# Optimization experiments

Hardware: AMD Instinct MI355X
Metric: run time of the kernel (lower is better)

Reference implementation:

```python
import jax, jax.numpy as jnp
import numpy as np

B, T, D = 2, 2048, 2048
N_HEADS, N_KV, HEAD_DIM = 8, 4, 256
S_CACHE = 2048
WINDOW = 512
SOFT_CAP = 50.0
ROPE_TS = 10000
ROPE_PROP = 1.0
EPS = 1e-6
NEG_INF = -2.3819763e38


def setup_inputs() -> dict:
    key = jax.random.key(0)
    ks = jax.random.split(key, 6)
    x = jax.random.normal(ks[0], (B, T, D), dtype=jnp.float32)
    wq = jax.random.normal(ks[1], (D, N_HEADS * HEAD_DIM), dtype=jnp.float32) * (D ** -0.5)
    wk = jax.random.normal(ks[2], (D, N_KV * HEAD_DIM), dtype=jnp.float32) * (D ** -0.5)
    wv = jax.random.normal(ks[3], (D, N_KV * HEAD_DIM), dtype=jnp.float32) * (D ** -0.5)
    wo = jax.random.normal(ks[4], (N_HEADS * HEAD_DIM, D), dtype=jnp.float32) * ((N_HEADS * HEAD_DIM) ** -0.5)
    return {
        'x': x,
        'segment_pos': jnp.broadcast_to(jnp.arange(T, dtype=jnp.int32), (B, T)),
        'cur_ind': 0,
        'wq': wq, 'wk': wk, 'wv': wv, 'wo': wo,
        'q_norm_scale': jnp.zeros((HEAD_DIM,), jnp.float32),
        'k_norm_scale': jnp.zeros((HEAD_DIM,), jnp.float32),
        'k_cache': jnp.zeros((B, S_CACHE, N_KV, HEAD_DIM), jnp.float32),
        'v_cache': jnp.zeros((B, S_CACHE, N_KV, HEAD_DIM), jnp.float32),
    }


def _rms_norm(x, scale, eps=EPS):
    # Gemma4RMSNorm: fp32 norm, (1 + scale) offset
    xf = x.astype(jnp.float32)
    n = xf * jax.lax.rsqrt(jnp.mean(jnp.square(xf), -1, keepdims=True) + eps)
    return (n * (1.0 + scale)).astype(x.dtype)


def _apply_rope(x, pos, max_timescale=ROPE_TS, proportion=ROPE_PROP):
    # x: [B, T, n, H]; pos: [B, T]. Partial RoPE on first proportion*H dims.
    H = x.shape[-1]
    rope_dim = int(H * proportion)
    half = rope_dim // 2
    frac = jnp.arange(half, dtype=jnp.float32) / half
    timescale = jnp.asarray(max_timescale, jnp.float32) ** frac  # [half]
    sinusoid = pos.astype(jnp.float32)[..., None] / timescale    # [B, T, half]
    sin = jnp.sin(sinusoid)[:, :, None, :]
    cos = jnp.cos(sinusoid)[:, :, None, :]
    x_rope, x_pass = x[..., :rope_dim], x[..., rope_dim:]
    x1, x2 = x_rope[..., :half], x_rope[..., half:]
    rotated = jnp.concatenate([x1 * cos - x2 * sin, x2 * cos + x1 * sin], axis=-1)
    return jnp.concatenate([rotated, x_pass], axis=-1).astype(x.dtype)


def reference(x, segment_pos, cur_ind, wq, wk, wv, wo, q_norm_scale, k_norm_scale, k_cache, v_cache):
    b, t, _ = x.shape
    g = N_HEADS // N_KV  # GQA group size

    q = (x @ wq).reshape(b, t, N_HEADS, HEAD_DIM)
    k = (x @ wk).reshape(b, t, N_KV, HEAD_DIM)
    v = (x @ wv).reshape(b, t, N_KV, HEAD_DIM)

    # QK-norm (per-head RMSNorm) then RoPE
    q = _rms_norm(q, q_norm_scale)
    k = _rms_norm(k, k_norm_scale)
    q = _apply_rope(q, segment_pos)
    k = _apply_rope(k, segment_pos)

    # KV-cache scatter write at cur_ind
    idx = jnp.asarray(cur_ind, jnp.int32)
    k_cache = jax.lax.dynamic_update_slice(k_cache, k, (0, idx, 0, 0))
    v_cache = jax.lax.dynamic_update_slice(v_cache, v, (0, idx, 0, 0))

    # Attention logits over full cache: [b, kv, g, t, s]
    qg = q.reshape(b, t, N_KV, g, HEAD_DIM) * (HEAD_DIM ** -0.5)
    logits = jnp.einsum('btkgh,bskh->bkgts', qg, k_cache)
    logits = SOFT_CAP * jnp.tanh(logits / SOFT_CAP)

    # Causal + sliding-window mask from absolute positions
    q_pos = segment_pos[:, :, None]                              # [b, t, 1]
    k_pos = jnp.arange(S_CACHE, dtype=jnp.int32)[None, None, :]  # [1, 1, s]
    mask = (k_pos <= q_pos) & (q_pos - k_pos < WINDOW)           # [b, t, s]
    logits = jnp.where(mask[:, None, None, :, :], logits, NEG_INF)

    probs = jax.nn.softmax(logits, axis=-1)
    attn = jnp.einsum('bkgts,bskh->btkgh', probs, v_cache).reshape(b, t, N_HEADS * HEAD_DIM)
    return attn @ wo
```

## Files before the change

kernel.cpp:

```cpp
#include <hip/hip_runtime.h>

#define T_SEQ 2048
#define NHEADS 8
#define NKV 4
#define HD 256
#define WIN 512

typedef __bf16 bf16x8 __attribute__((ext_vector_type(8)));
typedef float f32x4 __attribute__((ext_vector_type(4)));

__device__ __forceinline__ float bf2f(unsigned short u) {
    return __uint_as_float(((unsigned int)u) << 16);
}
__device__ __forceinline__ unsigned short f2bf(float f) {
    unsigned int u = __float_as_uint(f);
    u += 0x7fffu + ((u >> 16) & 1u);
    return (unsigned short)(u >> 16);
}

#define GLOAD_LDS16(gptr, lptr)                                            \
    __builtin_amdgcn_global_load_lds(                                      \
        (const __attribute__((address_space(1))) unsigned int*)(gptr),     \
        (__attribute__((address_space(3))) unsigned int*)(lptr), 16, 0, 0)

__global__ void detect_dtype(const unsigned short* __restrict__ x, int* flag) {
    int tid = threadIdx.x;
    int cnt = 0;
    for (int i = 0; i < 64; ++i) {
        unsigned short u = x[2 * (tid * 64 + i)];
        int e = (u >> 7) & 0xFF;
        cnt += (e >= 100 && e <= 140) ? 1 : 0;
    }
    #pragma unroll
    for (int o = 32; o >= 1; o >>= 1) cnt += __shfl_xor(cnt, o);
    if (tid == 0) *flag = (cnt > 2048) ? 1 : 0;
}

__global__ __launch_bounds__(256) void convert_to_bf16(
    const void* __restrict__ src, unsigned short* __restrict__ dst,
    const int* __restrict__ flag, int n)
{
    int i = (blockIdx.x * 256 + threadIdx.x) * 8;
    if (i >= n) return;
    if (*flag) {
        *(uint4*)&dst[i] = *(const uint4*)((const unsigned short*)src + i);
    } else {
        const float* s = (const float*)src + i;
        unsigned short v[8];
        #pragma unroll
        for (int j = 0; j < 8; ++j) v[j] = f2bf(s[j]);
        *(uint4*)&dst[i] = *(uint4*)v;
    }
}

__global__ __launch_bounds__(256) void transpose_cvt(
    const void* __restrict__ src, unsigned short* __restrict__ dst,
    const int* __restrict__ flag, int R, int C)
{
    __shared__ unsigned short tile[32][33];
    const int t = threadIdx.x;
    const int c = t & 31, r8 = t >> 5;
    const int bx = blockIdx.x, by = blockIdx.y;
    const int isb = *flag;
    #pragma unroll
    for (int i = 0; i < 4; ++i) {
        int r = r8 + i * 8;
        size_t idx = (size_t)(by * 32 + r) * C + bx * 32 + c;
        tile[r][c] = isb ? ((const unsigned short*)src)[idx]
                         : f2bf(((const float*)src)[idx]);
    }
    __syncthreads();
    #pragma unroll
    for (int i = 0; i < 4; ++i) {
        int r = r8 + i * 8;
        dst[(size_t)(bx * 32 + r) * R + by * 32 + c] = tile[c][r];
    }
}

__global__ __launch_bounds__(256) void transpose_qkv_w(
    const void* __restrict__ wq, const void* __restrict__ wk,
    const void* __restrict__ wv, unsigned short* __restrict__ dst,
    const int* __restrict__ flag)
{
    __shared__ unsigned short tile[32][33];
    const int t = threadIdx.x;
    const int c = t & 31, r8 = t >> 5;
    const int bx = blockIdx.x, by = blockIdx.y;
    const void* src; int C, rowoff, cb;
    if (bx < 64)      { src = wq; C = 2048; rowoff = 0;    cb = bx; }
    else if (bx < 96) { src = wk; C = 1024; rowoff = 2048; cb = bx - 64; }
    else              { src = wv; C = 1024; rowoff = 3072; cb = bx - 96; }
    const int isb = *flag;
    #pragma unroll
    for (int i = 0; i < 4; ++i) {
        int r = r8 + i * 8;
        size_t idx = (size_t)(by * 32 + r) * C + cb * 32 + c;
        tile[r][c] = isb ? ((const unsigned short*)src)[idx]
                         : f2bf(((const float*)src)[idx]);
    }
    __syncthreads();
    #pragma unroll
    for (int i = 0; i < 4; ++i) {
        int r = r8 + i * 8;
        dst[(size_t)(rowoff + cb * 32 + r) * 2048 + by * 32 + c] = tile[c][r];
    }
}

__global__ __launch_bounds__(256) void gemm_bf16(
    const unsigned short* __restrict__ A,
    const unsigned short* __restrict__ Bt,
    void* __restrict__ C,
    int M, int Ntot, int K, int n_base,
    const int* __restrict__ flag, int force_bf16)
{
    __shared__ __align__(16) unsigned short As[128 * 32];
    __shared__ __align__(16) unsigned short Bs[128 * 32];
    const int tid = threadIdx.x;
    const int n0 = blockIdx.x * 128;
    const int m0 = blockIdx.y * 128;
    const int wave = tid >> 6;
    const int lane = tid & 63;
    const int wm = (wave >> 1) * 64;
    const int wn = (wave & 1) * 64;
    const int quad = lane >> 4;
    const int l16 = lane & 15;
    const int obf = force_bf16 | *flag;

    f32x4 acc[4][4];
    #pragma unroll
    for (int i = 0; i < 4; ++i)
        #pragma unroll
        for (int j = 0; j < 4; ++j)
            acc[i][j] = f32x4{0.f, 0.f, 0.f, 0.f};

    for (int kk = 0; kk < K; kk += 32) {
        #pragma unroll
        for (int i = 0; i < 2; ++i) {
            int ch = tid + i * 256;
            int row = ch >> 2;
            int ko = (ch & 3) * 8;
            GLOAD_LDS16(&A[(size_t)(m0 + row) * K + kk + ko],  &As[ch * 8]);
            GLOAD_LDS16(&Bt[(size_t)(n0 + row) * K + kk + ko], &Bs[ch * 8]);
        }
        __syncthreads();
        bf16x8 af[4], bfr[4];
        #pragma unroll
        for (int mi = 0; mi < 4; ++mi)
            af[mi] = *(const bf16x8*)&As[(wm + mi * 16 + l16) * 32 + quad * 8];
        #pragma unroll
        for (int ni = 0; ni < 4; ++ni)
            bfr[ni] = *(const bf16x8*)&Bs[(wn + ni * 16 + l16) * 32 + quad * 8];
        #pragma unroll
        for (int mi = 0; mi < 4; ++mi)
            #pragma unroll
            for (int ni = 0; ni < 4; ++ni)
                acc[mi][ni] = __builtin_amdgcn_mfma_f32_16x16x32_bf16(
                    af[mi], bfr[ni], acc[mi][ni], 0, 0, 0);
        __syncthreads();
    }

    #pragma unroll
    for (int mi = 0; mi < 4; ++mi)
        #pragma unroll
        for (int ni = 0; ni < 4; ++ni)
            #pragma unroll
            for (int r = 0; r < 4; ++r) {
                int row = m0 + wm + mi * 16 + quad * 4 + r;
                int col = n_base + n0 + wn + ni * 16 + l16;
                size_t idx = (size_t)row * Ntot + col;
                if (obf) ((unsigned short*)C)[idx] = f2bf(acc[mi][ni][r]);
                else     ((float*)C)[idx]          = acc[mi][ni][r];
            }
}

__global__ __launch_bounds__(512, 2) void gemm256_bf16(
    const unsigned short* __restrict__ A,
    const unsigned short* __restrict__ Bt,
    void* __restrict__ C,
    int M, int Ntot, int K, int n_base, int gx,
    const int* __restrict__ flag, int force_bf16)
{
    __shared__ __align__(16) unsigned short A_lds[2][256 * 64];
    __shared__ __align__(16) unsigned short B_lds[2][256 * 64];

    const int tid = threadIdx.x;
    const int cpx = gridDim.x >> 3;
    const int swzb = (blockIdx.x & 7) * cpx + (blockIdx.x >> 3);
    const int bx = swzb % gx, by = swzb / gx;
    const int n0 = bx * 256, m0 = by * 256;

    const int wave = tid >> 6, lane = tid & 63;
    const int wr = wave >> 2, wc = wave & 3;
    const int quad = lane >> 4, l16 = lane & 15;
    const int sw7 = l16 & 7;
    const int obf = force_bf16 | *flag;

    const int trow = tid >> 3;
    const int tg   = tid & 7;
    const int tsw  = (tg ^ (trow & 7)) * 8;

    f32x4 acc[8][4];
    #pragma unroll
    for (int i = 0; i < 8; ++i)
        #pragma unroll
        for (int j = 0; j < 4; ++j)
            acc[i][j] = f32x4{0.f, 0.f, 0.f, 0.f};

    const int NT = K >> 6;
    const int NI = NT >> 1;

#define STAGE_A(d_, hm_, kt_)                                                  \
    do { _Pragma("unroll") for (int j = 0; j < 2; ++j) {                       \
        int r_ = j * 128 + (hm_) * 64 + trow;                                  \
        GLOAD_LDS16(&A[(size_t)(m0 + r_) * K + (kt_) * 64 + tsw],              \
                    &A_lds[d_][((hm_) * 128 + j * 64 + trow) * 64 + tg * 8]);  \
    } } while (0)

#define STAGE_B(d_, hn_, kt_)                                                  \
    do { _Pragma("unroll") for (int j = 0; j < 2; ++j) {                       \
        int w2_ = j * 64 + trow;                                               \
        int r_ = (w2_ >> 5) * 64 + (hn_) * 32 + (w2_ & 31);                    \
        GLOAD_LDS16(&Bt[(size_t)(n0 + r_) * K + (kt_) * 64 + tsw],             \
                    &B_lds[d_][((hn_) * 128 + w2_) * 64 + tg * 8]);            \
    } } while (0)

    bf16x8 a[4][2], b0[2][2], b1[2][2];

#define LDA_H(d_, hm_)                                                         \
    do { _Pragma("unroll") for (int mi = 0; mi < 4; ++mi)                      \
         _Pragma("unroll") for (int ks = 0; ks < 2; ++ks)                      \
            a[mi][ks] = *(const bf16x8*)&A_lds[d_][                            \
                ((hm_) * 128 + wr * 64 + mi * 16 + l16) * 64                   \
                + (((ks * 4 + quad) ^ sw7) * 8)]; } while (0)

#define LDB_H(d_, hn_, bb_)                                                    \
    do { _Pragma("unroll") for (int ni = 0; ni < 2; ++ni)                      \
         _Pragma("unroll") for (int ks = 0; ks < 2; ++ks)                      \
            bb_[ni][ks] = *(const bf16x8*)&B_lds[d_][                          \
                ((hn_) * 128 + wc * 32 + ni * 16 + l16) * 64                   \
                + (((ks * 4 + quad) ^ sw7) * 8)]; } while (0)

#define MFMAQ(hm_, hn_, bb_)                                                   \
    do { __builtin_amdgcn_s_setprio(1);                                        \
         _Pragma("unroll") for (int mi = 0; mi < 4; ++mi)                      \
         _Pragma("unroll") for (int ni = 0; ni < 2; ++ni)                      \
         _Pragma("unroll") for (int ks = 0; ks < 2; ++ks)                      \
            acc[(hm_) * 4 + mi][(hn_) * 2 + ni] =                              \
                __builtin_amdgcn_mfma_f32_16x16x32_bf16(                       \
                    a[mi][ks], bb_[ni][ks],                                    \
                    acc[(hm_) * 4 + mi][(hn_) * 2 + ni], 0, 0, 0);             \
         __builtin_amdgcn_s_setprio(0); } while (0)

#define BAR() do { __builtin_amdgcn_sched_barrier(0);                          \
                   __builtin_amdgcn_s_barrier();                               \
                   __builtin_amdgcn_sched_barrier(0); } while (0)
#define LGKM0() do { asm volatile("s_waitcnt lgkmcnt(0)" ::: "memory");        \
                     __builtin_amdgcn_sched_barrier(0); } while (0)
#define VMC(n_) asm volatile("s_waitcnt vmcnt(" #n_ ")" ::: "memory")

    STAGE_A(0, 0, 0); STAGE_B(0, 0, 0); STAGE_B(0, 1, 0); STAGE_A(0, 1, 0);
    STAGE_A(1, 0, 1); STAGE_B(1, 0, 1); STAGE_B(1, 1, 1);
    VMC(6);
    BAR();

    for (int i = 0; i < NI; ++i) {
        const int t2 = 2 * i + 2, t3 = 2 * i + 3;
        const bool s2 = t2 < NT, s3 = t3 < NT;

        LDA_H(0, 0); LDB_H(0, 0, b0);
        STAGE_A(1, 1, 2 * i + 1);
        BAR(); LGKM0(); MFMAQ(0, 0, b0);
        BAR();
        LDB_H(0, 1, b1);
        if (s2) STAGE_A(0, 0, t2);
        BAR(); LGKM0(); MFMAQ(0, 1, b1);
        BAR();
        LDA_H(0, 1);
        if (s2) STAGE_B(0, 0, t2);
        BAR(); LGKM0(); MFMAQ(1, 1, b1);
        BAR();
        if (s2) STAGE_B(0, 1, t2);
        BAR(); LGKM0(); MFMAQ(1, 0, b0);
        if (s2) { VMC(6); } else { VMC(0); }
        BAR();
        LDA_H(1, 0); LDB_H(1, 0, b0);
        if (s2) STAGE_A(0, 1, t2);
        BAR(); LGKM0(); MFMAQ(0, 0, b0);
        BAR();
        LDB_H(1, 1, b1);
        if (s3) STAGE_A(1, 0, t3);
        BAR(); LGKM0(); MFMAQ(0, 1, b1);
        BAR();
        LDA_H(1, 1);
        if (s3) STAGE_B(1, 0, t3);
        BAR(); LGKM0(); MFMAQ(1, 1, b1);
        BAR();
        if (s3) STAGE_B(1, 1, t3);
        BAR(); LGKM0(); MFMAQ(1, 0, b0);
        if (s3) { VMC(6); } else { VMC(0); }
        BAR();
    }

#undef STAGE_A
#undef STAGE_B
#undef LDA_H
#undef LDB_H
#undef MFMAQ
#undef BAR
#undef LGKM0
#undef VMC

    #pragma unroll
    for (int mi = 0; mi < 8; ++mi)
        #pragma unroll
        for (int ni = 0; ni < 4; ++ni)
            #pragma unroll
            for (int r = 0; r < 4; ++r) {
                int row = m0 + wr * 128 + mi * 16 + quad * 4 + r;
                int col = n_base + n0 + wc * 64 + ni * 16 + l16;
                size_t idx = (size_t)row * Ntot + col;
                if (obf) ((unsigned short*)C)[idx] = f2bf(acc[mi][ni][r]);
                else     ((float*)C)[idx]          = acc[mi][ni][r];
            }
}

__global__ __launch_bounds__(256) void finalize_qk(
    unsigned short* __restrict__ qkv,
    const int* __restrict__ segment_pos,
    const void* __restrict__ qs_raw,
    const void* __restrict__ ks_raw,
    const int* __restrict__ flag)
{
    const int w = blockIdx.x * 4 + (threadIdx.x >> 6);
    const int lane = threadIdx.x & 63;
    const int b = w / (T_SEQ * 12);
    const int rem = w % (T_SEQ * 12);
    const int t = rem / 12;
    const int slot = rem % 12;
    const bool isq = slot < 8;
    const int col0 = isq ? slot * 256 : 2048 + (slot - 8) * 256;
    unsigned short* p = qkv + (size_t)(b * T_SEQ + t) * 4096 + col0;
    const int isb = *flag;

    float e[4];
    #pragma unroll
    for (int j = 0; j < 4; ++j) e[j] = bf2f(p[lane + 64 * j]);
    float ss = e[0] * e[0] + e[1] * e[1] + e[2] * e[2] + e[3] * e[3];
    #pragma unroll
    for (int o = 32; o >= 1; o >>= 1) ss += __shfl_xor(ss, o);
    const float rn = rsqrtf(ss * (1.0f / 256.0f) + 1e-6f);
    const void* scp = isq ? qs_raw : ks_raw;
    float nrm[4];
    #pragma unroll
    for (int j = 0; j < 4; ++j) {
        float sc = isb ? bf2f(((const unsigned short*)scp)[lane + 64 * j])
                       : ((const float*)scp)[lane + 64 * j];
        nrm[j] = e[j] * rn * (1.0f + sc);
    }

    const int pos = segment_pos[b * T_SEQ + t];
    #pragma unroll
    for (int pp = 0; pp < 2; ++pp) {
        const int i = lane + 64 * pp;
        const float inv_ts = __expf((float)i * -0.07195578415606293f);
        float s, c;
        __sincosf((float)pos * inv_ts, &s, &c);
        const float x1 = nrm[pp], x2 = nrm[pp + 2];
        p[i]       = f2bf(x1 * c - x2 * s);
        p[i + 128] = f2bf(x2 * c + x1 * s);
    }
}

__global__ __launch_bounds__(256) void build_vt(
    const unsigned short* __restrict__ qkv, unsigned short* __restrict__ vt)
{
    __shared__ unsigned short tile[32][33];
    const int bkv = blockIdx.z;
    const int b = bkv >> 2, kv = bkv & 3;
    const int s0 = blockIdx.x * 32, d0 = blockIdx.y * 32;
    const int c = threadIdx.x & 31, r8 = threadIdx.x >> 5;
    #pragma unroll
    for (int i = 0; i < 4; ++i) {
        int r = r8 + i * 8;
        tile[r][c] = qkv[(size_t)(b * T_SEQ + s0 + r) * 4096 + 3072 + kv * 256 + d0 + c];
    }
    __syncthreads();
    #pragma unroll
    for (int i = 0; i < 4; ++i) {
        int r = r8 + i * 8;
        vt[((size_t)bkv * 256 + d0 + r) * T_SEQ + s0 + c] = tile[c][r];
    }
}

#define PSTR 80
__global__ __launch_bounds__(256, 2) void attn_mfma(
    const unsigned short* __restrict__ qkv,
    const unsigned short* __restrict__ vt,
    unsigned short* __restrict__ out)
{
    __shared__ __align__(16) unsigned short SMEM[16384 + 16384 + 4 * 16 * PSTR];
    unsigned short* K_lds  = SMEM;
    unsigned short* VT_lds = SMEM + 16384;

    const int tid = threadIdx.x;
    const int wave = tid >> 6, lane = tid & 63;
    const int l16 = lane & 15, quad = lane >> 4;
    const int sw = l16 & 7;
    const int bkv = blockIdx.x & 7;
    const int qt  = blockIdx.x >> 3;
    const int b = bkv >> 2, kvh = bkv & 3;
    const int t0 = qt * 32;
    const int h = kvh * 2 + (wave >> 1);
    const int woff = (wave & 1) * 16;
    const int tq = t0 + woff + l16;
    unsigned short* P_lds = SMEM + 32768 + wave * 16 * PSTR;

    bf16x8 qf[8];
    {
        const unsigned short* qp =
            qkv + (size_t)(b * T_SEQ + tq) * 4096 + h * 256 + quad * 8;
        #pragma unroll
        for (int c = 0; c < 8; ++c) qf[c] = *(const bf16x8*)(qp + 32 * c);
    }

    f32x4 o[16];
    #pragma unroll
    for (int nt = 0; nt < 16; ++nt) o[nt] = f32x4{0.f, 0.f, 0.f, 0.f};
    float l_run = 0.f;

    int s_lo = t0 - (WIN - 1); if (s_lo < 0) s_lo = 0;
    const int s_base = s_lo & ~63;
    const int s_last = t0 + 31;
    const int tqmin = t0 + woff;
    const int tqmax = tqmin + 15;
    const int wlo   = tqmin - (WIN - 1);
    const size_t kgbase = (size_t)b * T_SEQ * 4096 + 2048 + kvh * 256;
    const size_t vgbase = (size_t)bkv * 256 * T_SEQ;

    for (int sb = s_base; sb <= s_last; sb += 64) {
        __syncthreads();

        #pragma unroll
        for (int i = 0; i < 8; ++i) {
            int ch = tid + 256 * i;
            int row = ch >> 5, e8 = ch & 31;
            GLOAD_LDS16(&qkv[kgbase + (size_t)(sb + row) * 4096
                             + ((e8 ^ (row & 7)) * 8)],
                        &K_lds[ch * 8]);
        }
        #pragma unroll
        for (int i = 0; i < 8; ++i) {
            int ch = tid + 256 * i;
            int dr = ch >> 3, e8 = ch & 7;
            GLOAD_LDS16(&vt[vgbase + (size_t)dr * T_SEQ + sb
                            + ((e8 ^ (dr & 7)) * 8)],
                        &VT_lds[ch * 8]);
        }
        __syncthreads();

        if (sb > tqmax || sb + 63 < wlo) continue;

        f32x4 st[4];
        #pragma unroll
        for (int mt = 0; mt < 4; ++mt) st[mt] = f32x4{0.f, 0.f, 0.f, 0.f};
        __builtin_amdgcn_s_setprio(1);
        #pragma unroll
        for (int c = 0; c < 8; ++c) {
            bf16x8 kf[4];
            #pragma unroll
            for (int mt = 0; mt < 4; ++mt)
                kf[mt] = *(const bf16x8*)&K_lds[(mt * 16 + l16) * 256 + (((4 * c + quad) ^ sw) * 8)];
            #pragma unroll
            for (int mt = 0; mt < 4; ++mt)
                st[mt] = __builtin_amdgcn_mfma_f32_16x16x32_bf16(kf[mt], qf[c], st[mt], 0, 0, 0);
        }
        __builtin_amdgcn_s_setprio(0);

        #pragma unroll
        for (int mt = 0; mt < 4; ++mt)
            #pragma unroll
            for (int r = 0; r < 4; ++r) {
                int sp = sb + mt * 16 + quad * 4 + r;
                float e2 = __expf(st[mt][r] * 0.0025f);
                float p = __expf(20.0f - 100.0f / (e2 + 1.0f));
                bool valid = (sp <= tq) && (tq - sp < WIN);
                p = valid ? p : 0.0f;
                l_run += p;
                P_lds[l16 * PSTR + mt * 16 + quad * 4 + r] = f2bf(p);
            }

        #pragma unroll
        for (int c = 0; c < 2; ++c) {
            bf16x8 pf = *(const bf16x8*)&P_lds[l16 * PSTR + 32 * c + quad * 8];
            __builtin_amdgcn_s_setprio(1);
            #pragma unroll
            for (int nt = 0; nt < 16; ++nt) {
                bf16x8 vf = *(const bf16x8*)&VT_lds[(nt * 16 + l16) * 64 + (((4 * c + quad) ^ sw) * 8)];
                o[nt] = __builtin_amdgcn_mfma_f32_16x16x32_bf16(pf, vf, o[nt], 0, 0, 0);
            }
            __builtin_amdgcn_s_setprio(0);
        }
    }

    l_run += __shfl_xor(l_run, 16);
    l_run += __shfl_xor(l_run, 32);
    float linv[4];
    #pragma unroll
    for (int r = 0; r < 4; ++r) linv[r] = 1.0f / __shfl(l_run, quad * 4 + r);

    __syncthreads();
    unsigned short* W = SMEM + wave * (16 * 264);
    #pragma unroll
    for (int nt = 0; nt < 16; ++nt)
        #pragma unroll
        for (int r = 0; r < 4; ++r)
            W[(quad * 4 + r) * 264 + nt * 16 + l16] = f2bf(o[nt][r] * linv[r]);
    const int lr = lane >> 2, lc = (lane & 3) * 64;
    unsigned short* ob = out + (size_t)(b * T_SEQ + t0 + woff + lr) * 2048 + h * 256 + lc;
    #pragma unroll
    for (int j = 0; j < 8; ++j)
        *(uint4*)(ob + j * 8) = *(const uint4*)&W[lr * 264 + lc + j * 8];
}

extern "C" void kernel_launch(void* const* d_in, const int* in_sizes, int n_in,
                              void* d_out, int out_size, void* d_ws, size_t ws_size,
                              hipStream_t stream) {
    const void* x   = d_in[0];
    const int*  sp  = (const int*)d_in[1];
    const void* wq  = d_in[3];
    const void* wk  = d_in[4];
    const void* wv  = d_in[5];
    const void* wo  = d_in[6];
    const void* qsc = d_in[7];
    const void* ksc = d_in[8];

    unsigned short* ws = (unsigned short*)d_ws;
    int*            flag = (int*)ws;
    unsigned short* qkv  = (unsigned short*)d_out;
    dim3 blk(256);

    const size_t NEED = (size_t)(2048 + 8388608 + 8388608) * sizeof(unsigned short);

    detect_dtype<<<1, 64, 0, stream>>>((const unsigned short*)x, flag);

    if (ws_size >= NEED) {
        unsigned short* xhat = ws + 2048;
        unsigned short* wT   = xhat + (size_t)4096 * 2048;
        unsigned short* abuf = xhat;
        unsigned short* vtb  = wT;
        unsigned short* woT  = wT + (size_t)2048 * 2048;

        convert_to_bf16<<<4096, blk, 0, stream>>>(x, xhat, flag, 4096 * 2048);

        transpose_qkv_w<<<dim3(128, 64), blk, 0, stream>>>(wq, wk, wv, wT, flag);

        gemm256_bf16<<<256, 512, 0, stream>>>(xhat, wT, qkv,
                                              4096, 4096, 2048, 0, 16, flag, 1);

        finalize_qk<<<12288, blk, 0, stream>>>(qkv, sp, qsc, ksc, flag);

        build_vt<<<dim3(64, 8, 8), blk, 0, stream>>>(qkv, vtb);
        attn_mfma<<<512, blk, 0, stream>>>(qkv, vtb, abuf);

        transpose_cvt<<<dim3(64, 64), blk, 0, stream>>>(wo, woT, flag, 2048, 2048);
        gemm256_bf16<<<128, 512, 0, stream>>>(abuf, woT, d_out,
                                              4096, 2048, 2048, 0, 8, flag, 0);
    } else {
        unsigned short* reg1 = ws + 2048;
        unsigned short* reg2 = reg1 + (size_t)4096 * 2048;
        unsigned short* xhat = reg1;
        unsigned short* abuf = reg1;

        convert_to_bf16<<<4096, blk, 0, stream>>>(x, xhat, flag, 4096 * 2048);

        transpose_cvt<<<dim3(64, 64), blk, 0, stream>>>(wq, reg2, flag, 2048, 2048);
        gemm_bf16<<<dim3(16, 32), blk, 0, stream>>>(xhat, reg2, qkv,
                                                    4096, 4096, 2048, 0, flag, 1);
        transpose_cvt<<<dim3(32, 64), blk, 0, stream>>>(wk, reg2,                     flag, 2048, 1024);
        transpose_cvt<<<dim3(32, 64), blk, 0, stream>>>(wv, reg2 + (size_t)1024*2048, flag, 2048, 1024);
        gemm_bf16<<<dim3(16, 32), blk, 0, stream>>>(xhat, reg2, qkv,
                                                    4096, 4096, 2048, 2048, flag, 1);

        finalize_qk<<<12288, blk, 0, stream>>>(qkv, sp, qsc, ksc, flag);

        build_vt<<<dim3(64, 8, 8), blk, 0, stream>>>(qkv, reg2);
        attn_mfma<<<512, blk, 0, stream>>>(qkv, reg2, abuf);

        transpose_cvt<<<dim3(64, 64), blk, 0, stream>>>(wo, reg2, flag, 2048, 2048);
        gemm_bf16<<<dim3(16, 32), blk, 0, stream>>>(abuf, reg2, d_out,
                                                    4096, 2048, 2048, 0, flag, 0);
    }
}
```

Before: 359.1 us.

## Fuse prep/post kernels and overlap V loads with QK compute in attention

Merges the input conversion with the QKV weight transpose into one launch. It also merges QK-norm/RoPE, the V transpose and the wo transpose into a second launch, cutting kernel launches and tail effects between small kernels. In the attention loop, the kernel now waits only for the K tile (partial vmcnt) before computing QK logits, and waits for the V tile later. This lets V global-to-LDS loads overlap the QK MFMAs and softmax. Inactive tiles now still run the barriers. Correctness depends on the vmcnt count matching the load issue order.

```diff
diff --git a/kernel.cpp b/kernel.cpp
--- a/kernel.cpp
+++ b/kernel.cpp
@@ -36,13 +36,10 @@
     if (tid == 0) *flag = (cnt > 2048) ? 1 : 0;
 }
 
-__global__ __launch_bounds__(256) void convert_to_bf16(
-    const void* __restrict__ src, unsigned short* __restrict__ dst,
-    const int* __restrict__ flag, int n)
-{
-    int i = (blockIdx.x * 256 + threadIdx.x) * 8;
-    if (i >= n) return;
-    if (*flag) {
+__device__ __forceinline__ void dev_convert8(
+    const void* src, unsigned short* dst, int isb, int i)
+{
+    if (isb) {
         *(uint4*)&dst[i] = *(const uint4*)((const unsigned short*)src + i);
     } else {
         const float* s = (const float*)src + i;
@@ -53,15 +50,11 @@
     }
 }
 
-__global__ __launch_bounds__(256) void transpose_cvt(
-    const void* __restrict__ src, unsigned short* __restrict__ dst,
-    const int* __restrict__ flag, int R, int C)
-{
-    __shared__ unsigned short tile[32][33];
-    const int t = threadIdx.x;
-    const int c = t & 31, r8 = t >> 5;
-    const int bx = blockIdx.x, by = blockIdx.y;
-    const int isb = *flag;
+__device__ __forceinline__ void dev_transpose32(
+    const void* src, unsigned short* dst, int isb, int R, int C,
+    int bx, int by, int tid, unsigned short (*tile)[33])
+{
+    const int c = tid & 31, r8 = tid >> 5;
     #pragma unroll
     for (int i = 0; i < 4; ++i) {
         int r = r8 + i * 8;
@@ -77,32 +70,150 @@
     }
 }
 
-__global__ __launch_bounds__(256) void transpose_qkv_w(
-    const void* __restrict__ wq, const void* __restrict__ wk,
-    const void* __restrict__ wv, unsigned short* __restrict__ dst,
-    const int* __restrict__ flag)
-{
-    __shared__ unsigned short tile[32][33];
-    const int t = threadIdx.x;
-    const int c = t & 31, r8 = t >> 5;
-    const int bx = blockIdx.x, by = blockIdx.y;
-    const void* src; int C, rowoff, cb;
-    if (bx < 64)      { src = wq; C = 2048; rowoff = 0;    cb = bx; }
-    else if (bx < 96) { src = wk; C = 1024; rowoff = 2048; cb = bx - 64; }
-    else              { src = wv; C = 1024; rowoff = 3072; cb = bx - 96; }
-    const int isb = *flag;
+__device__ __forceinline__ void dev_finalize(
+    unsigned short* qkv, const int* segment_pos,
+    const void* qs_raw, const void* ks_raw, int isb, int w, int lane)
+{
+    const int b = w / (T_SEQ * 12);
+    const int rem = w % (T_SEQ * 12);
+    const int t = rem / 12;
+    const int slot = rem % 12;
+    const bool isq = slot < 8;
+    const int col0 = isq ? slot * 256 : 2048 + (slot - 8) * 256;
+    unsigned short* p = qkv + (size_t)(b * T_SEQ + t) * 4096 + col0;
+
+    float e[4];
+    #pragma unroll
+    for (int j = 0; j < 4; ++j) e[j] = bf2f(p[lane + 64 * j]);
+    float ss = e[0] * e[0] + e[1] * e[1] + e[2] * e[2] + e[3] * e[3];
+    #pragma unroll
+    for (int o = 32; o >= 1; o >>= 1) ss += __shfl_xor(ss, o);
+    const float rn = rsqrtf(ss * (1.0f / 256.0f) + 1e-6f);
+    const void* scp = isq ? qs_raw : ks_raw;
+    float nrm[4];
+    #pragma unroll
+    for (int j = 0; j < 4; ++j) {
+        float sc = isb ? bf2f(((const unsigned short*)scp)[lane + 64 * j])
+                       : ((const float*)scp)[lane + 64 * j];
+        nrm[j] = e[j] * rn * (1.0f + sc);
+    }
+
+    const int pos = segment_pos[b * T_SEQ + t];
+    #pragma unroll
+    for (int pp = 0; pp < 2; ++pp) {
+        const int i = lane + 64 * pp;
+        const float inv_ts = __expf((float)i * -0.07195578415606293f);
+        float s, c;
+        __sincosf((float)pos * inv_ts, &s, &c);
+        const float x1 = nrm[pp], x2 = nrm[pp + 2];
+        p[i]       = f2bf(x1 * c - x2 * s);
+        p[i + 128] = f2bf(x2 * c + x1 * s);
+    }
+}
+
+__device__ __forceinline__ void dev_build_vt(
+    const unsigned short* qkv, unsigned short* vt,
+    int bx, int by, int bz, int tid, unsigned short (*tile)[33])
+{
+    const int bkv = bz;
+    const int b = bkv >> 2, kv = bkv & 3;
+    const int s0 = bx * 32, d0 = by * 32;
+    const int c = tid & 31, r8 = tid >> 5;
     #pragma unroll
     for (int i = 0; i < 4; ++i) {
         int r = r8 + i * 8;
-        size_t idx = (size_t)(by * 32 + r) * C + cb * 32 + c;
-        tile[r][c] = isb ? ((const unsigned short*)src)[idx]
-                         : f2bf(((const float*)src)[idx]);
+        tile[r][c] = qkv[(size_t)(b * T_SEQ + s0 + r) * 4096 + 3072 + kv * 256 + d0 + c];
     }
     __syncthreads();
     #pragma unroll
     for (int i = 0; i < 4; ++i) {
         int r = r8 + i * 8;
-        dst[(size_t)(rowoff + cb * 32 + r) * 2048 + by * 32 + c] = tile[c][r];
+        vt[((size_t)bkv * 256 + d0 + r) * T_SEQ + s0 + c] = tile[c][r];
+    }
+}
+
+__global__ __launch_bounds__(256) void convert_to_bf16(
+    const void* __restrict__ src, unsigned short* __restrict__ dst,
+    const int* __restrict__ flag, int n)
+{
+    int i = (blockIdx.x * 256 + threadIdx.x) * 8;
+    if (i >= n) return;
+    dev_convert8(src, dst, *flag, i);
+}
+
+__global__ __launch_bounds__(256) void transpose_cvt(
+    const void* __restrict__ src, unsigned short* __restrict__ dst,
+    const int* __restrict__ flag, int R, int C)
+{
+    __shared__ unsigned short tile[32][33];
+    dev_transpose32(src, dst, *flag, R, C, blockIdx.x, blockIdx.y,
+                    threadIdx.x, tile);
+}
+
+__global__ __launch_bounds__(256) void finalize_qk(
+    unsigned short* __restrict__ qkv,
+    const int* __restrict__ segment_pos,
+    const void* __restrict__ qs_raw,
+    const void* __restrict__ ks_raw,
+    const int* __restrict__ flag)
+{
+    dev_finalize(qkv, segment_pos, qs_raw, ks_raw, *flag,
+                 blockIdx.x * 4 + (threadIdx.x >> 6), threadIdx.x & 63);
+}
+
+__global__ __launch_bounds__(256) void build_vt(
+    const unsigned short* __restrict__ qkv, unsigned short* __restrict__ vt)
+{
+    __shared__ unsigned short tile[32][33];
+    dev_build_vt(qkv, vt, blockIdx.x, blockIdx.y, blockIdx.z,
+                 threadIdx.x, tile);
+}
+
+__global__ __launch_bounds__(256) void prep_fused(
+    const void* __restrict__ x,
+    const void* __restrict__ wq, const void* __restrict__ wk,
+    const void* __restrict__ wv,
+    unsigned short* __restrict__ xhat, unsigned short* __restrict__ wT,
+    const int* __restrict__ flag)
+{
+    __shared__ unsigned short tile[32][33];
+    const int bid = blockIdx.x;
+    const int tid = threadIdx.x;
+    const int isb = *flag;
+    if (bid < 4096) {
+        dev_convert8(x, xhat, isb, (bid * 256 + tid) * 8);
+    } else {
+        const int k = bid - 4096;
+        const int bx = k % 128, by = k / 128;
+        const void* src; int C, rowoff, cb;
+        if (bx < 64)      { src = wq; C = 2048; rowoff = 0;    cb = bx; }
+        else if (bx < 96) { src = wk; C = 1024; rowoff = 2048; cb = bx - 64; }
+        else              { src = wv; C = 1024; rowoff = 3072; cb = bx - 96; }
+        dev_transpose32(src, wT + (size_t)rowoff * 2048, isb, 2048, C,
+                        cb, by, tid, tile);
+    }
+}
+
+__global__ __launch_bounds__(256) void post_fused(
+    unsigned short* __restrict__ qkv,
+    const int* __restrict__ segment_pos,
+    const void* __restrict__ qs_raw, const void* __restrict__ ks_raw,
+    unsigned short* __restrict__ vt,
+    const void* __restrict__ wo, unsigned short* __restrict__ woT,
+    const int* __restrict__ flag)
+{
+    __shared__ unsigned short tile[32][33];
+    const int bid = blockIdx.x;
+    const int tid = threadIdx.x;
+    if (bid < 12288) {
+        dev_finalize(qkv, segment_pos, qs_raw, ks_raw, *flag,
+                     bid * 4 + (tid >> 6), tid & 63);
+    } else if (bid < 16384) {
+        const int k = bid - 12288;
+        dev_build_vt(qkv, vt, k % 64, (k / 64) % 8, k / 512, tid, tile);
+    } else {
+        const int k = bid - 16384;
+        dev_transpose32(wo, woT, *flag, 2048, 2048, k % 64, k / 64, tid, tile);
     }
 }
 
@@ -324,75 +435,10 @@
             }
 }
 
-__global__ __launch_bounds__(256) void finalize_qk(
-    unsigned short* __restrict__ qkv,
-    const int* __restrict__ segment_pos,
-    const void* __restrict__ qs_raw,
-    const void* __restrict__ ks_raw,
-    const int* __restrict__ flag)
-{
-    const int w = blockIdx.x * 4 + (threadIdx.x >> 6);
-    const int lane = threadIdx.x & 63;
-    const int b = w / (T_SEQ * 12);
-    const int rem = w % (T_SEQ * 12);
-    const int t = rem / 12;
-    const int slot = rem % 12;
-    const bool isq = slot < 8;
-    const int col0 = isq ? slot * 256 : 2048 + (slot - 8) * 256;
-    unsigned short* p = qkv + (size_t)(b * T_SEQ + t) * 4096 + col0;
-    const int isb = *flag;
-
-    float e[4];
-    #pragma unroll
-    for (int j = 0; j < 4; ++j) e[j] = bf2f(p[lane + 64 * j]);
-    float ss = e[0] * e[0] + e[1] * e[1] + e[2] * e[2] + e[3] * e[3];
-    #pragma unroll
-    for (int o = 32; o >= 1; o >>= 1) ss += __shfl_xor(ss, o);
-    const float rn = rsqrtf(ss * (1.0f / 256.0f) + 1e-6f);
-    const void* scp = isq ? qs_raw : ks_raw;
-    float nrm[4];
-    #pragma unroll
-    for (int j = 0; j < 4; ++j) {
-        float sc = isb ? bf2f(((const unsigned short*)scp)[lane + 64 * j])
-                       : ((const float*)scp)[lane + 64 * j];
-        nrm[j] = e[j] * rn * (1.0f + sc);
-    }
-
-    const int pos = segment_pos[b * T_SEQ + t];
-    #pragma unroll
-    for (int pp = 0; pp < 2; ++pp) {
-        const int i = lane + 64 * pp;
-        const float inv_ts = __expf((float)i * -0.07195578415606293f);
-        float s, c;
-        __sincosf((float)pos * inv_ts, &s, &c);
-        const float x1 = nrm[pp], x2 = nrm[pp + 2];
-        p[i]       = f2bf(x1 * c - x2 * s);
-        p[i + 128] = f2bf(x2 * c + x1 * s);
-    }
-}
-
-__global__ __launch_bounds__(256) void build_vt(
-    const unsigned short* __restrict__ qkv, unsigned short* __restrict__ vt)
-{
-    __shared__ unsigned short tile[32][33];
-    const int bkv = blockIdx.z;
-    const int b = bkv >> 2, kv = bkv & 3;
-    const int s0 = blockIdx.x * 32, d0 = blockIdx.y * 32;
-    const int c = threadIdx.x & 31, r8 = threadIdx.x >> 5;
-    #pragma unroll
-    for (int i = 0; i < 4; ++i) {
-        int r = r8 + i * 8;
-        tile[r][c] = qkv[(size_t)(b * T_SEQ + s0 + r) * 4096 + 3072 + kv * 256 + d0 + c];
-    }
-    __syncthreads();
-    #pragma unroll
-    for (int i = 0; i < 4; ++i) {
-        int r = r8 + i * 8;
-        vt[((size_t)bkv * 256 + d0 + r) * T_SEQ + s0 + c] = tile[c][r];
-    }
-}
-
 #define PSTR 80
+#define ABAR() do { __builtin_amdgcn_sched_barrier(0);                         \
+                    __builtin_amdgcn_s_barrier();                              \
+                    __builtin_amdgcn_sched_barrier(0); } while (0)
 __global__ __launch_bounds__(256, 2) void attn_mfma(
     const unsigned short* __restrict__ qkv,
     const unsigned short* __restrict__ vt,
@@ -438,7 +484,7 @@
     const size_t vgbase = (size_t)bkv * 256 * T_SEQ;
 
     for (int sb = s_base; sb <= s_last; sb += 64) {
-        __syncthreads();
+        ABAR();
 
         #pragma unroll
         for (int i = 0; i < 8; ++i) {
@@ -456,49 +502,57 @@
                             + ((e8 ^ (dr & 7)) * 8)],
                         &VT_lds[ch * 8]);
         }
-        __syncthreads();
-
-        if (sb > tqmax || sb + 63 < wlo) continue;
+        asm volatile("s_waitcnt vmcnt(8)" ::: "memory");
+        ABAR();
+
+        const bool act = !(sb > tqmax || sb + 63 < wlo);
 
         f32x4 st[4];
         #pragma unroll
         for (int mt = 0; mt < 4; ++mt) st[mt] = f32x4{0.f, 0.f, 0.f, 0.f};
-        __builtin_amdgcn_s_setprio(1);
-        #pragma unroll
-        for (int c = 0; c < 8; ++c) {
-            bf16x8 kf[4];
+        if (act) {
+            __builtin_amdgcn_s_setprio(1);
+            #pragma unroll
+            for (int c = 0; c < 8; ++c) {
+                bf16x8 kf[4];
+                #pragma unroll
+                for (int mt = 0; mt < 4; ++mt)
+                    kf[mt] = *(const bf16x8*)&K_lds[(mt * 16 + l16) * 256 + (((4 * c + quad) ^ sw) * 8)];
+                #pragma unroll
+                for (int mt = 0; mt < 4; ++mt)
+                    st[mt] = __builtin_amdgcn_mfma_f32_16x16x32_bf16(kf[mt], qf[c], st[mt], 0, 0, 0);
+            }
+            __builtin_amdgcn_s_setprio(0);
+
             #pragma unroll
             for (int mt = 0; mt < 4; ++mt)
-                kf[mt] = *(const bf16x8*)&K_lds[(mt * 16 + l16) * 256 + (((4 * c + quad) ^ sw) * 8)];
+                #pragma unroll
+                for (int r = 0; r < 4; ++r) {
+                    int sp = sb + mt * 16 + quad * 4 + r;
+                    float e2 = __expf(st[mt][r] * 0.0025f);
+                    float p = __expf(20.0f - 100.0f / (e2 + 1.0f));
+                    bool valid = (sp <= tq) && (tq - sp < WIN);
+                    p = valid ? p : 0.0f;
+                    l_run += p;
+                    P_lds[l16 * PSTR + mt * 16 + quad * 4 + r] = f2bf(p);
+                }
+        }
+
+        asm volatile("s_waitcnt vmcnt(0)" ::: "memory");
+        ABAR();
+
+        if (act) {
             #pragma unroll
-            for (int mt = 0; mt < 4; ++mt)
-                st[mt] = __builtin_amdgcn_mfma_f32_16x16x32_bf16(kf[mt], qf[c], st[mt], 0, 0, 0);
-        }
-        __builtin_amdgcn_s_setprio(0);
-
-        #pragma unroll
-        for (int mt = 0; mt < 4; ++mt)
-            #pragma unroll
-            for (int r = 0; r < 4; ++r) {
-                int sp = sb + mt * 16 + quad * 4 + r;
-                float e2 = __expf(st[mt][r] * 0.0025f);
-                float p = __expf(20.0f - 100.0f / (e2 + 1.0f));
-                bool valid = (sp <= tq) && (tq - sp < WIN);
-                p = valid ? p : 0.0f;
-                l_run += p;
-                P_lds[l16 * PSTR + mt * 16 + quad * 4 + r] = f2bf(p);
+            for (int c = 0; c < 2; ++c) {
+                bf16x8 pf = *(const bf16x8*)&P_lds[l16 * PSTR + 32 * c + quad * 8];
+                __builtin_amdgcn_s_setprio(1);
+                #pragma unroll
+                for (int nt = 0; nt < 16; ++nt) {
+                    bf16x8 vf = *(const bf16x8*)&VT_lds[(nt * 16 + l16) * 64 + (((4 * c + quad) ^ sw) * 8)];
+                    o[nt] = __builtin_amdgcn_mfma_f32_16x16x32_bf16(pf, vf, o[nt], 0, 0, 0);
+                }
+                __builtin_amdgcn_s_setprio(0);
             }
-
-        #pragma unroll
-        for (int c = 0; c < 2; ++c) {
-            bf16x8 pf = *(const bf16x8*)&P_lds[l16 * PSTR + 32 * c + quad * 8];
-            __builtin_amdgcn_s_setprio(1);
-            #pragma unroll
-            for (int nt = 0; nt < 16; ++nt) {
-                bf16x8 vf = *(const bf16x8*)&VT_lds[(nt * 16 + l16) * 64 + (((4 * c + quad) ^ sw) * 8)];
-                o[nt] = __builtin_amdgcn_mfma_f32_16x16x32_bf16(pf, vf, o[nt], 0, 0, 0);
-            }
-            __builtin_amdgcn_s_setprio(0);
         }
     }
 
@@ -550,19 +604,15 @@
         unsigned short* vtb  = wT;
         unsigned short* woT  = wT + (size_t)2048 * 2048;
 
-        convert_to_bf16<<<4096, blk, 0, stream>>>(x, xhat, flag, 4096 * 2048);
-
-        transpose_qkv_w<<<dim3(128, 64), blk, 0, stream>>>(wq, wk, wv, wT, flag);
+        prep_fused<<<12288, blk, 0, stream>>>(x, wq, wk, wv, xhat, wT, flag);
 
         gemm256_bf16<<<256, 512, 0, stream>>>(xhat, wT, qkv,
                                               4096, 4096, 2048, 0, 16, flag, 1);
 
-        finalize_qk<<<12288, blk, 0, stream>>>(qkv, sp, qsc, ksc, flag);
-
-        build_vt<<<dim3(64, 8, 8), blk, 0, stream>>>(qkv, vtb);
+        post_fused<<<20480, blk, 0, stream>>>(qkv, sp, qsc, ksc, vtb, wo, woT, flag);
+
         attn_mfma<<<512, blk, 0, stream>>>(qkv, vtb, abuf);
 
-        transpose_cvt<<<dim3(64, 64), blk, 0, stream>>>(wo, woT, flag, 2048, 2048);
         gemm256_bf16<<<128, 512, 0, stream>>>(abuf, woT, d_out,
                                               4096, 2048, 2048, 0, 8, flag, 0);
     } else {
```

Result: faster. 350.9 us (-2.3%).
